# Kernel optimization log

Measured on AMD Instinct MI355X. Metric: run time of the kernel, lower is better.

Reference implementation:

```python
import jax, jax.numpy as jnp
import numpy as np

N = 262144   # occupied sparse voxels
C = 64       # channels
K3 = 27      # 3^3 kernel offsets (rulebook width)


def spconv(feats, W, nbr):
    """Submanifold sparse conv: gather -> matmul -> accumulate per kernel offset.
    feats: [N, Cin], W: [K3, Cin, Cout], nbr: [N, K3] int32 neighbor indices.
    """
    def step(acc, wi):
        w, idx = wi          # w: [Cin, Cout], idx: [N]
        return acc + feats[idx] @ w, None
    acc = jnp.zeros((feats.shape[0], W.shape[-1]), dtype=feats.dtype)
    out, _ = jax.lax.scan(step, acc, (W, nbr.T))
    return out


def inr(feats, nbr, w00, w01, w10, w11, w12):
    # branch 0: conv0_1(relu(conv0_0(x)))  (both k=3)
    out0 = spconv(jax.nn.relu(spconv(feats, w00, nbr)), w01, nbr)
    # branch 1: conv1_2(relu(conv1_1(relu(conv1_0(x)))))  (1x1, k=3, 1x1)
    out1 = jax.nn.relu(spconv(jax.nn.relu(feats @ w10), w11, nbr)) @ w12
    # concat halves back to C, residual add
    return jnp.concatenate([out0, out1], axis=1) + feats


def setup_inputs() -> dict:
    key = jax.random.key(0)
    ks = jax.random.split(key, 16)
    Ch = C // 2
    s3 = 1.0 / np.sqrt(K3 * C)
    s3h = 1.0 / np.sqrt(K3 * Ch)
    s1 = 1.0 / np.sqrt(C)
    s1h = 1.0 / np.sqrt(Ch)
    feats = jax.random.normal(ks[0], (N, C), dtype=jnp.float32)
    nbr = jax.random.randint(ks[1], (N, K3), 0, N, dtype=jnp.int32)
    w1 = jax.random.normal(ks[2], (K3, C, C), dtype=jnp.float32) * s3
    w2 = jax.random.normal(ks[3], (K3, C, C), dtype=jnp.float32) * s3
    # 3 stacked INR blocks
    b00 = jax.random.normal(ks[4], (3, K3, C, Ch), dtype=jnp.float32) * s3
    b01 = jax.random.normal(ks[5], (3, K3, Ch, Ch), dtype=jnp.float32) * s3h
    b10 = jax.random.normal(ks[6], (3, C, Ch), dtype=jnp.float32) * s1
    b11 = jax.random.normal(ks[7], (3, K3, Ch, Ch), dtype=jnp.float32) * s3h
    b12 = jax.random.normal(ks[8], (3, Ch, Ch), dtype=jnp.float32) * s1h
    return {"feats": feats, "nbr": nbr, "w1": w1, "w2": w2,
            "b00": b00, "b01": b01, "b10": b10, "b11": b11, "b12": b12}


def reference(feats, nbr, w1, w2, b00, b01, b10, b11, b12):
    x = jax.nn.relu(spconv(feats, w1, nbr))   # x = relu(conv1(x))
    h = x
    for i in range(3):
        h = inr(h, nbr, b00[i], b01[i], b10[i], b11[i], b12[i])
    out = h + x                                # block(x) + x
    return spconv(out, w2, nbr)                # conv2(out)
```

## Files before the change

kernel.cpp:

```cpp
#include <hip/hip_runtime.h>
#include <hip/hip_bf16.h>

typedef __attribute__((ext_vector_type(8))) __bf16 bf16x8;
typedef __attribute__((ext_vector_type(4))) float f32x4;

#define DEVI __device__ __forceinline__

static constexpr int NVOX = 262144;

DEVI unsigned short f2b_rne(float f) {
    unsigned int u = __float_as_uint(f);
    u = (u + 0x7fffu + ((u >> 16) & 1u)) >> 16;
    return (unsigned short)u;
}
DEVI float b2f(unsigned short h) {
    return __uint_as_float(((unsigned int)h) << 16);
}
DEVI bf16x8 ld8(const unsigned short* p) { return *reinterpret_cast<const bf16x8*>(p); }
DEVI f32x4 mfma16(bf16x8 a, bf16x8 b, f32x4 c) {
    return __builtin_amdgcn_mfma_f32_16x16x32_bf16(a, b, c, 0, 0, 0);
}

DEVI void stage16(const unsigned short* __restrict__ src, unsigned short* dst,
                  int n16, int tid, int nthr) {
    const float4* s = reinterpret_cast<const float4*>(src);
    float4* d = reinterpret_cast<float4*>(dst);
    for (int c = tid; c < n16; c += nthr) d[c] = s[c];
}


__global__ void f2b_kernel(const float* __restrict__ src, unsigned short* __restrict__ dst) {
    const size_t i = (size_t)(blockIdx.x * 256 + threadIdx.x) * 8;
    const float4 a = *reinterpret_cast<const float4*>(src + i);
    const float4 b = *reinterpret_cast<const float4*>(src + i + 4);
    union { unsigned short h[8]; uint4 v; } o;
    o.h[0] = f2b_rne(a.x); o.h[1] = f2b_rne(a.y); o.h[2] = f2b_rne(a.z); o.h[3] = f2b_rne(a.w);
    o.h[4] = f2b_rne(b.x); o.h[5] = f2b_rne(b.y); o.h[6] = f2b_rne(b.z); o.h[7] = f2b_rne(b.w);
    *reinterpret_cast<uint4*>(dst + i) = o.v;
}

__global__ void wconv_kernel(const float* __restrict__ src, unsigned short* __restrict__ dst,
                             int K, int Cin, int Cout) {
    const int KC = Cin >> 5, NT = Cout >> 4;
    const int total = K * KC * NT * 512;
    src += (size_t)blockIdx.y * K * Cin * Cout;
    dst += (size_t)blockIdx.y * total;
    for (int e = blockIdx.x * 256 + threadIdx.x; e < total; e += gridDim.x * 256) {
        const int j = e & 7;
        const int ln = (e >> 3) & 63;
        const int blob = e >> 9;
        const int nt = blob % NT;
        const int t = blob / NT;
        const int kc = t % KC;
        const int k = t / KC;
        const int cin = kc * 32 + (ln >> 4) * 8 + j;
        const int cout = nt * 16 + (ln & 15);
        dst[e] = f2b_rne(src[((size_t)k * Cin + cin) * Cout + cout]);
    }
}


template<bool RELU, bool OUTF32>
__global__ __launch_bounds__(1024)
void conv_full_kernel(const unsigned short* __restrict__ in,
                      const int* __restrict__ nbr,
                      const unsigned short* __restrict__ wf,
                      void* __restrict__ outv)
{
    __shared__ unsigned short wlds[14 * 8 * 512];
    const int tid = threadIdx.x;
    const int lane = tid & 63, wave = tid >> 6;
    const int lrow = lane & 15, lkg = lane >> 4;
    const int vb = blockIdx.x * 512 + wave * 32;

    const f32x4 FZ = {0.f, 0.f, 0.f, 0.f};
    f32x4 acc[2][4];
#pragma unroll
    for (int m = 0; m < 2; ++m)
#pragma unroll
        for (int nt = 0; nt < 4; ++nt) acc[m][nt] = FZ;

#pragma unroll 1
    for (int stage = 0; stage < 2; ++stage) {
        const int k0 = stage * 14;
        const int nk = stage ? 13 : 14;
        __syncthreads();
        stage16(wf + (size_t)k0 * 8 * 512, wlds, nk * 8 * 64, tid, 1024);
        __syncthreads();
#pragma unroll 1
        for (int kk = 0; kk < nk; ++kk) {
            const int k = k0 + kk;
            const int idx0 = nbr[(vb + lrow) * 27 + k];
            const int idx1 = nbr[(vb + 16 + lrow) * 27 + k];
            const unsigned short* a0 = in + (size_t)idx0 * 64;
            const unsigned short* a1 = in + (size_t)idx1 * 64;
            const unsigned short* bl = wlds + kk * 8 * 512 + lane * 8;
#pragma unroll
            for (int kc = 0; kc < 2; ++kc) {
                const bf16x8 af0 = ld8(a0 + kc * 32 + lkg * 8);
                const bf16x8 af1 = ld8(a1 + kc * 32 + lkg * 8);
#pragma unroll
                for (int nt = 0; nt < 4; ++nt) {
                    const bf16x8 bf = ld8(bl + (kc * 4 + nt) * 512);
                    acc[0][nt] = mfma16(af0, bf, acc[0][nt]);
                    acc[1][nt] = mfma16(af1, bf, acc[1][nt]);
                }
            }
        }
    }

#pragma unroll
    for (int m = 0; m < 2; ++m)
#pragma unroll
        for (int nt = 0; nt < 4; ++nt)
#pragma unroll
            for (int r = 0; r < 4; ++r) {
                const int v = vb + m * 16 + lkg * 4 + r;
                float val = acc[m][nt][r];
                if (RELU) val = fmaxf(val, 0.f);
                if (OUTF32)
                    reinterpret_cast<float*>(outv)[(size_t)v * 64 + nt * 16 + lrow] = val;
                else
                    reinterpret_cast<unsigned short*>(outv)[(size_t)v * 64 + nt * 16 + lrow] = f2b_rne(val);
            }
}

__global__ __launch_bounds__(1024)
void kernel_A(const unsigned short* __restrict__ h,
              const int* __restrict__ nbr,
              const unsigned short* __restrict__ b00f,
              const unsigned short* __restrict__ b10f,
              unsigned short* __restrict__ u)
{
    __shared__ unsigned short wlds[(27 * 4 + 4) * 512];
    const int tid = threadIdx.x;
    const int lane = tid & 63, wave = tid >> 6;
    const int lrow = lane & 15, lkg = lane >> 4;
    const int vb = blockIdx.x * 512 + wave * 32;

    stage16(b00f, wlds, 27 * 4 * 64, tid, 1024);
    stage16(b10f, wlds + 27 * 4 * 512, 4 * 64, tid, 1024);
    __syncthreads();

    const f32x4 FZ = {0.f, 0.f, 0.f, 0.f};
    f32x4 acc0[2][2], acc1[2][2];
#pragma unroll
    for (int m = 0; m < 2; ++m)
#pragma unroll
        for (int nt = 0; nt < 2; ++nt) { acc0[m][nt] = FZ; acc1[m][nt] = FZ; }

#pragma unroll 1
    for (int k = 0; k < 27; ++k) {
        const int idx0 = nbr[(vb + lrow) * 27 + k];
        const int idx1 = nbr[(vb + 16 + lrow) * 27 + k];
        const unsigned short* a0 = h + (size_t)idx0 * 64;
        const unsigned short* a1 = h + (size_t)idx1 * 64;
        const unsigned short* bl = wlds + k * 4 * 512 + lane * 8;
#pragma unroll
        for (int kc = 0; kc < 2; ++kc) {
            const bf16x8 af0 = ld8(a0 + kc * 32 + lkg * 8);
            const bf16x8 af1 = ld8(a1 + kc * 32 + lkg * 8);
#pragma unroll
            for (int nt = 0; nt < 2; ++nt) {
                const bf16x8 bf = ld8(bl + (kc * 2 + nt) * 512);
                acc0[0][nt] = mfma16(af0, bf, acc0[0][nt]);
                acc0[1][nt] = mfma16(af1, bf, acc0[1][nt]);
            }
        }
    }
    {
        const unsigned short* bl = wlds + 27 * 4 * 512 + lane * 8;
#pragma unroll
        for (int m = 0; m < 2; ++m) {
            const unsigned short* ar = h + (size_t)(vb + m * 16 + lrow) * 64;
#pragma unroll
            for (int kc = 0; kc < 2; ++kc) {
                const bf16x8 af = ld8(ar + kc * 32 + lkg * 8);
#pragma unroll
                for (int nt = 0; nt < 2; ++nt) {
                    const bf16x8 bf = ld8(bl + (kc * 2 + nt) * 512);
                    acc1[m][nt] = mfma16(af, bf, acc1[m][nt]);
                }
            }
        }
    }
#pragma unroll
    for (int m = 0; m < 2; ++m)
#pragma unroll
        for (int nt = 0; nt < 2; ++nt)
#pragma unroll
            for (int r = 0; r < 4; ++r) {
                const int v = vb + m * 16 + lkg * 4 + r;
                u[(size_t)v * 64 + nt * 16 + lrow] = f2b_rne(fmaxf(acc0[m][nt][r], 0.f));
                u[(size_t)v * 64 + 32 + nt * 16 + lrow] = f2b_rne(fmaxf(acc1[m][nt][r], 0.f));
            }
}

__global__ __launch_bounds__(1024)
void kernel_B(const unsigned short* __restrict__ u,
              const int* __restrict__ nbr,
              const unsigned short* __restrict__ b01f,
              const unsigned short* __restrict__ b11f,
              const unsigned short* __restrict__ b12f,
              const unsigned short* __restrict__ hres,
              const unsigned short* __restrict__ xres,
              unsigned short* __restrict__ hout)
{
    __shared__ unsigned short wlds[110 * 512];
    __shared__ unsigned short t2lds[16][512];
    const int tid = threadIdx.x;
    const int lane = tid & 63, wave = tid >> 6;
    const int lrow = lane & 15, lkg = lane >> 4;
    const int vb = blockIdx.x * 512 + wave * 32;

    stage16(b01f, wlds, 54 * 64, tid, 1024);
    stage16(b11f, wlds + 54 * 512, 54 * 64, tid, 1024);
    stage16(b12f, wlds + 108 * 512, 2 * 64, tid, 1024);
    __syncthreads();

    const f32x4 FZ = {0.f, 0.f, 0.f, 0.f};
    f32x4 acc0[2][2], acc1[2][2];
#pragma unroll
    for (int m = 0; m < 2; ++m)
#pragma unroll
        for (int nt = 0; nt < 2; ++nt) { acc0[m][nt] = FZ; acc1[m][nt] = FZ; }

#pragma unroll 1
    for (int k = 0; k < 27; ++k) {
        const int idx0 = nbr[(vb + lrow) * 27 + k];
        const int idx1 = nbr[(vb + 16 + lrow) * 27 + k];
        const unsigned short* a0 = u + (size_t)idx0 * 64;
        const unsigned short* a1 = u + (size_t)idx1 * 64;
        const bf16x8 af00 = ld8(a0 + lkg * 8);
        const bf16x8 af01 = ld8(a0 + 32 + lkg * 8);
        const bf16x8 af10 = ld8(a1 + lkg * 8);
        const bf16x8 af11 = ld8(a1 + 32 + lkg * 8);
        const unsigned short* bl = wlds + lane * 8;
#pragma unroll
        for (int nt = 0; nt < 2; ++nt) {
            const bf16x8 w01 = ld8(bl + (k * 2 + nt) * 512);
            const bf16x8 w11 = ld8(bl + (54 + k * 2 + nt) * 512);
            acc0[0][nt] = mfma16(af00, w01, acc0[0][nt]);
            acc0[1][nt] = mfma16(af10, w01, acc0[1][nt]);
            acc1[0][nt] = mfma16(af01, w11, acc1[0][nt]);
            acc1[1][nt] = mfma16(af11, w11, acc1[1][nt]);
        }
    }

    f32x4 out1[2][2];
    char* tb = reinterpret_cast<char*>(&t2lds[wave][0]);
#pragma unroll
    for (int m = 0; m < 2; ++m) {
#pragma unroll
        for (int nt = 0; nt < 2; ++nt)
#pragma unroll
            for (int r = 0; r < 4; ++r) {
                const int row = lkg * 4 + r;
                const int byte = (nt * 16 + lrow) * 2;
                const int off = row * 64 + (((byte >> 4) ^ (row & 3)) << 4) + (byte & 15);
                *reinterpret_cast<unsigned short*>(tb + off) = f2b_rne(fmaxf(acc1[m][nt][r], 0.f));
            }
        __syncthreads();
        const int roff = lrow * 64 + ((lkg ^ (lrow & 3)) << 4);
        const bf16x8 af2 = *reinterpret_cast<const bf16x8*>(tb + roff);
#pragma unroll
        for (int nt = 0; nt < 2; ++nt) {
            const bf16x8 w12 = ld8(wlds + (108 + nt) * 512 + lane * 8);
            out1[m][nt] = mfma16(af2, w12, FZ);
        }
        __syncthreads();
    }

#pragma unroll
    for (int m = 0; m < 2; ++m)
#pragma unroll
        for (int nt = 0; nt < 2; ++nt)
#pragma unroll
            for (int r = 0; r < 4; ++r) {
                const int v = vb + m * 16 + lkg * 4 + r;
                const int c0 = nt * 16 + lrow;
                const int c1 = 32 + c0;
                float r0 = acc0[m][nt][r] + b2f(hres[(size_t)v * 64 + c0]);
                float r1 = out1[m][nt][r] + b2f(hres[(size_t)v * 64 + c1]);
                if (xres) {
                    r0 += b2f(xres[(size_t)v * 64 + c0]);
                    r1 += b2f(xres[(size_t)v * 64 + c1]);
                }
                hout[(size_t)v * 64 + c0] = f2b_rne(r0);
                hout[(size_t)v * 64 + c1] = f2b_rne(r1);
            }
}


extern "C" void kernel_launch(void* const* d_in, const int* in_sizes, int n_in,
                              void* d_out, int out_size, void* d_ws, size_t ws_size,
                              hipStream_t stream)
{
    const float* feats = (const float*)d_in[0];
    const int*   nbr   = (const int*)d_in[1];
    const float* w1    = (const float*)d_in[2];
    const float* w2    = (const float*)d_in[3];
    const float* b00   = (const float*)d_in[4];
    const float* b01   = (const float*)d_in[5];
    const float* b10   = (const float*)d_in[6];
    const float* b11   = (const float*)d_in[7];
    const float* b12   = (const float*)d_in[8];

    const size_t NC = (size_t)NVOX * 64;
    unsigned short* xbuf = (unsigned short*)d_ws;
    unsigned short* hbuf = xbuf + NC;
    unsigned short* wbuf = hbuf + NC;
    if (ws_size < (2 * NC + 562176) * sizeof(unsigned short)) return;

    unsigned short* fbuf = (unsigned short*)d_out;
    unsigned short* ubuf = fbuf + NC;

    const size_t OFF_W1 = 0, OFF_W2 = 110592, OFF_B00 = 221184, OFF_B01 = 387072,
                 OFF_B10 = 470016, OFF_B11 = 476160, OFF_B12 = 559104;

    f2b_kernel<<<8192, 256, 0, stream>>>(feats, fbuf);
    wconv_kernel<<<dim3(432, 1), 256, 0, stream>>>(w1, wbuf + OFF_W1, 27, 64, 64);
    wconv_kernel<<<dim3(432, 1), 256, 0, stream>>>(w2, wbuf + OFF_W2, 27, 64, 64);
    wconv_kernel<<<dim3(216, 3), 256, 0, stream>>>(b00, wbuf + OFF_B00, 27, 64, 32);
    wconv_kernel<<<dim3(108, 3), 256, 0, stream>>>(b01, wbuf + OFF_B01, 27, 32, 32);
    wconv_kernel<<<dim3(8, 3),   256, 0, stream>>>(b10, wbuf + OFF_B10, 1, 64, 32);
    wconv_kernel<<<dim3(108, 3), 256, 0, stream>>>(b11, wbuf + OFF_B11, 27, 32, 32);
    wconv_kernel<<<dim3(4, 3),   256, 0, stream>>>(b12, wbuf + OFF_B12, 1, 32, 32);

    conv_full_kernel<true, false><<<512, 1024, 0, stream>>>(fbuf, nbr, wbuf + OFF_W1, xbuf);

    for (int i = 0; i < 3; ++i) {
        kernel_A<<<512, 1024, 0, stream>>>(i ? hbuf : xbuf, nbr,
                                           wbuf + OFF_B00 + (size_t)i * 55296,
                                           wbuf + OFF_B10 + (size_t)i * 2048, ubuf);
        kernel_B<<<512, 1024, 0, stream>>>(ubuf, nbr,
                                           wbuf + OFF_B01 + (size_t)i * 27648,
                                           wbuf + OFF_B11 + (size_t)i * 27648,
                                           wbuf + OFF_B12 + (size_t)i * 1024,
                                           i ? hbuf : xbuf,
                                           (i == 2) ? xbuf : (const unsigned short*)nullptr,
                                           hbuf);
    }

    conv_full_kernel<false, true><<<512, 1024, 0, stream>>>(hbuf, nbr, wbuf + OFF_W2, d_out);
}
```

Measured before the change: 1.392 ms.

## Software-pipeline neighbor index and gather loads across kernel offsets

The three gather-conv kernels now fully unroll the 27-offset loop. Neighbor indices are prefetched 6 offsets ahead and gathered feature rows 2 offsets ahead, held in rotating register buffers. The first gathers are also issued before the LDS weight staging so global latency overlaps it. This targets the dependent index-then-gather latency chain that stalled each iteration, at the cost of higher register pressure in 1024-thread blocks, which could cause spills.

```diff
diff --git a/kernel.cpp b/kernel.cpp
--- a/kernel.cpp
+++ b/kernel.cpp
@@ -73,6 +73,27 @@
     const int lrow = lane & 15, lkg = lane >> 4;
     const int vb = blockIdx.x * 512 + wave * 32;
 
+    constexpr int ID = 6;
+    constexpr int GS = 3;
+
+    const int* nrow0 = nbr + (size_t)(vb + lrow) * 27;
+    const int* nrow1 = nbr + (size_t)(vb + 16 + lrow) * 27;
+
+    int i0[ID], i1[ID];
+    bf16x8 ga[GS][2][2];
+
+#pragma unroll
+    for (int t = 0; t < ID; ++t) { i0[t] = nrow0[t]; i1[t] = nrow1[t]; }
+#pragma unroll
+    for (int t = 0; t < 2; ++t) {
+        const unsigned short* a0 = in + (size_t)i0[t] * 64 + lkg * 8;
+        const unsigned short* a1 = in + (size_t)i1[t] * 64 + lkg * 8;
+        ga[t][0][0] = ld8(a0); ga[t][0][1] = ld8(a0 + 32);
+        ga[t][1][0] = ld8(a1); ga[t][1][1] = ld8(a1 + 32);
+    }
+
+    stage16(wf, wlds, 14 * 8 * 64, tid, 1024);
+
     const f32x4 FZ = {0.f, 0.f, 0.f, 0.f};
     f32x4 acc[2][4];
 #pragma unroll
@@ -80,33 +101,37 @@
 #pragma unroll
         for (int nt = 0; nt < 4; ++nt) acc[m][nt] = FZ;
 
-#pragma unroll 1
-    for (int stage = 0; stage < 2; ++stage) {
-        const int k0 = stage * 14;
-        const int nk = stage ? 13 : 14;
-        __syncthreads();
-        stage16(wf + (size_t)k0 * 8 * 512, wlds, nk * 8 * 64, tid, 1024);
-        __syncthreads();
-#pragma unroll 1
-        for (int kk = 0; kk < nk; ++kk) {
-            const int k = k0 + kk;
-            const int idx0 = nbr[(vb + lrow) * 27 + k];
-            const int idx1 = nbr[(vb + 16 + lrow) * 27 + k];
-            const unsigned short* a0 = in + (size_t)idx0 * 64;
-            const unsigned short* a1 = in + (size_t)idx1 * 64;
-            const unsigned short* bl = wlds + kk * 8 * 512 + lane * 8;
-#pragma unroll
-            for (int kc = 0; kc < 2; ++kc) {
-                const bf16x8 af0 = ld8(a0 + kc * 32 + lkg * 8);
-                const bf16x8 af1 = ld8(a1 + kc * 32 + lkg * 8);
-#pragma unroll
-                for (int nt = 0; nt < 4; ++nt) {
-                    const bf16x8 bf = ld8(bl + (kc * 4 + nt) * 512);
-                    acc[0][nt] = mfma16(af0, bf, acc[0][nt]);
-                    acc[1][nt] = mfma16(af1, bf, acc[1][nt]);
-                }
-            }
-        }
+    __syncthreads();
+
+#pragma unroll
+    for (int t = 0; t < 27; ++t) {
+        if (t == 14) {
+            __syncthreads();
+            stage16(wf + (size_t)14 * 8 * 512, wlds, 13 * 8 * 64, tid, 1024);
+            __syncthreads();
+        }
+        if (t + ID < 27) {
+            i0[t % ID] = nrow0[t + ID];
+            i1[t % ID] = nrow1[t + ID];
+        }
+        if (t + 2 < 27) {
+            const int u = t + 2, s = u % GS;
+            const unsigned short* a0 = in + (size_t)i0[u % ID] * 64 + lkg * 8;
+            const unsigned short* a1 = in + (size_t)i1[u % ID] * 64 + lkg * 8;
+            ga[s][0][0] = ld8(a0); ga[s][0][1] = ld8(a0 + 32);
+            ga[s][1][0] = ld8(a1); ga[s][1][1] = ld8(a1 + 32);
+        }
+        const int kk = (t < 14) ? t : t - 14;
+        const unsigned short* bl = wlds + kk * 8 * 512 + lane * 8;
+        const int s = t % GS;
+#pragma unroll
+        for (int kc = 0; kc < 2; ++kc)
+#pragma unroll
+            for (int nt = 0; nt < 4; ++nt) {
+                const bf16x8 bf = ld8(bl + (kc * 4 + nt) * 512);
+                acc[0][nt] = mfma16(ga[s][0][kc], bf, acc[0][nt]);
+                acc[1][nt] = mfma16(ga[s][1][kc], bf, acc[1][nt]);
+            }
     }
 
 #pragma unroll
@@ -138,9 +163,27 @@
     const int lrow = lane & 15, lkg = lane >> 4;
     const int vb = blockIdx.x * 512 + wave * 32;
 
+    constexpr int ID = 6;
+    constexpr int GS = 3;
+
+    const int* nrow0 = nbr + (size_t)(vb + lrow) * 27;
+    const int* nrow1 = nbr + (size_t)(vb + 16 + lrow) * 27;
+
+    int i0[ID], i1[ID];
+    bf16x8 ga[GS][2][2];
+
+#pragma unroll
+    for (int t = 0; t < ID; ++t) { i0[t] = nrow0[t]; i1[t] = nrow1[t]; }
+#pragma unroll
+    for (int t = 0; t < 2; ++t) {
+        const unsigned short* a0 = h + (size_t)i0[t] * 64 + lkg * 8;
+        const unsigned short* a1 = h + (size_t)i1[t] * 64 + lkg * 8;
+        ga[t][0][0] = ld8(a0); ga[t][0][1] = ld8(a0 + 32);
+        ga[t][1][0] = ld8(a1); ga[t][1][1] = ld8(a1 + 32);
+    }
+
     stage16(b00f, wlds, 27 * 4 * 64, tid, 1024);
     stage16(b10f, wlds + 27 * 4 * 512, 4 * 64, tid, 1024);
-    __syncthreads();
 
     const f32x4 FZ = {0.f, 0.f, 0.f, 0.f};
     f32x4 acc0[2][2], acc1[2][2];
@@ -149,24 +192,31 @@
 #pragma unroll
         for (int nt = 0; nt < 2; ++nt) { acc0[m][nt] = FZ; acc1[m][nt] = FZ; }
 
-#pragma unroll 1
-    for (int k = 0; k < 27; ++k) {
-        const int idx0 = nbr[(vb + lrow) * 27 + k];
-        const int idx1 = nbr[(vb + 16 + lrow) * 27 + k];
-        const unsigned short* a0 = h + (size_t)idx0 * 64;
-        const unsigned short* a1 = h + (size_t)idx1 * 64;
-        const unsigned short* bl = wlds + k * 4 * 512 + lane * 8;
-#pragma unroll
-        for (int kc = 0; kc < 2; ++kc) {
-            const bf16x8 af0 = ld8(a0 + kc * 32 + lkg * 8);
-            const bf16x8 af1 = ld8(a1 + kc * 32 + lkg * 8);
+    __syncthreads();
+
+#pragma unroll
+    for (int t = 0; t < 27; ++t) {
+        if (t + ID < 27) {
+            i0[t % ID] = nrow0[t + ID];
+            i1[t % ID] = nrow1[t + ID];
+        }
+        if (t + 2 < 27) {
+            const int u2 = t + 2, s = u2 % GS;
+            const unsigned short* a0 = h + (size_t)i0[u2 % ID] * 64 + lkg * 8;
+            const unsigned short* a1 = h + (size_t)i1[u2 % ID] * 64 + lkg * 8;
+            ga[s][0][0] = ld8(a0); ga[s][0][1] = ld8(a0 + 32);
+            ga[s][1][0] = ld8(a1); ga[s][1][1] = ld8(a1 + 32);
+        }
+        const unsigned short* bl = wlds + t * 4 * 512 + lane * 8;
+        const int s = t % GS;
+#pragma unroll
+        for (int kc = 0; kc < 2; ++kc)
 #pragma unroll
             for (int nt = 0; nt < 2; ++nt) {
                 const bf16x8 bf = ld8(bl + (kc * 2 + nt) * 512);
-                acc0[0][nt] = mfma16(af0, bf, acc0[0][nt]);
-                acc0[1][nt] = mfma16(af1, bf, acc0[1][nt]);
-            }
-        }
+                acc0[0][nt] = mfma16(ga[s][0][kc], bf, acc0[0][nt]);
+                acc0[1][nt] = mfma16(ga[s][1][kc], bf, acc0[1][nt]);
+            }
     }
     {
         const unsigned short* bl = wlds + 27 * 4 * 512 + lane * 8;
@@ -213,10 +263,28 @@
     const int lrow = lane & 15, lkg = lane >> 4;
     const int vb = blockIdx.x * 512 + wave * 32;
 
+    constexpr int ID = 6;
+    constexpr int GS = 3;
+
+    const int* nrow0 = nbr + (size_t)(vb + lrow) * 27;
+    const int* nrow1 = nbr + (size_t)(vb + 16 + lrow) * 27;
+
+    int i0[ID], i1[ID];
+    bf16x8 ga[GS][2][2];
+
+#pragma unroll
+    for (int t = 0; t < ID; ++t) { i0[t] = nrow0[t]; i1[t] = nrow1[t]; }
+#pragma unroll
+    for (int t = 0; t < 2; ++t) {
+        const unsigned short* a0 = u + (size_t)i0[t] * 64 + lkg * 8;
+        const unsigned short* a1 = u + (size_t)i1[t] * 64 + lkg * 8;
+        ga[t][0][0] = ld8(a0); ga[t][0][1] = ld8(a0 + 32);
+        ga[t][1][0] = ld8(a1); ga[t][1][1] = ld8(a1 + 32);
+    }
+
     stage16(b01f, wlds, 54 * 64, tid, 1024);
     stage16(b11f, wlds + 54 * 512, 54 * 64, tid, 1024);
     stage16(b12f, wlds + 108 * 512, 2 * 64, tid, 1024);
-    __syncthreads();
 
     const f32x4 FZ = {0.f, 0.f, 0.f, 0.f};
     f32x4 acc0[2][2], acc1[2][2];
@@ -225,25 +293,31 @@
 #pragma unroll
         for (int nt = 0; nt < 2; ++nt) { acc0[m][nt] = FZ; acc1[m][nt] = FZ; }
 
-#pragma unroll 1
-    for (int k = 0; k < 27; ++k) {
-        const int idx0 = nbr[(vb + lrow) * 27 + k];
-        const int idx1 = nbr[(vb + 16 + lrow) * 27 + k];
-        const unsigned short* a0 = u + (size_t)idx0 * 64;
-        const unsigned short* a1 = u + (size_t)idx1 * 64;
-        const bf16x8 af00 = ld8(a0 + lkg * 8);
-        const bf16x8 af01 = ld8(a0 + 32 + lkg * 8);
-        const bf16x8 af10 = ld8(a1 + lkg * 8);
-        const bf16x8 af11 = ld8(a1 + 32 + lkg * 8);
+    __syncthreads();
+
+#pragma unroll
+    for (int t = 0; t < 27; ++t) {
+        if (t + ID < 27) {
+            i0[t % ID] = nrow0[t + ID];
+            i1[t % ID] = nrow1[t + ID];
+        }
+        if (t + 2 < 27) {
+            const int u2 = t + 2, s = u2 % GS;
+            const unsigned short* a0 = u + (size_t)i0[u2 % ID] * 64 + lkg * 8;
+            const unsigned short* a1 = u + (size_t)i1[u2 % ID] * 64 + lkg * 8;
+            ga[s][0][0] = ld8(a0); ga[s][0][1] = ld8(a0 + 32);
+            ga[s][1][0] = ld8(a1); ga[s][1][1] = ld8(a1 + 32);
+        }
         const unsigned short* bl = wlds + lane * 8;
+        const int s = t % GS;
 #pragma unroll
         for (int nt = 0; nt < 2; ++nt) {
-            const bf16x8 w01 = ld8(bl + (k * 2 + nt) * 512);
-            const bf16x8 w11 = ld8(bl + (54 + k * 2 + nt) * 512);
-            acc0[0][nt] = mfma16(af00, w01, acc0[0][nt]);
-            acc0[1][nt] = mfma16(af10, w01, acc0[1][nt]);
-            acc1[0][nt] = mfma16(af01, w11, acc1[0][nt]);
-            acc1[1][nt] = mfma16(af11, w11, acc1[1][nt]);
+            const bf16x8 w01 = ld8(bl + (t * 2 + nt) * 512);
+            const bf16x8 w11 = ld8(bl + (54 + t * 2 + nt) * 512);
+            acc0[0][nt] = mfma16(ga[s][0][0], w01, acc0[0][nt]);
+            acc0[1][nt] = mfma16(ga[s][1][0], w01, acc0[1][nt]);
+            acc1[0][nt] = mfma16(ga[s][0][1], w11, acc1[0][nt]);
+            acc1[1][nt] = mfma16(ga[s][1][1], w11, acc1[1][nt]);
         }
     }
 
```

Result: faster. 1.174 ms (-15.6%).
